# Performance work log

Hardware: AMD Instinct MI355X
Metric: run time of the kernel (lower is better)

## Reference

```python
import jax, jax.numpy as jnp
import numpy as np

N_USERS = 100000
N_ITEMS = 50000
N = N_USERS + N_ITEMS
NNZ = 2400000
D = 64
L = 3
B = 16384


def setup_inputs() -> dict:
    key = jax.random.key(0)
    ks = jax.random.split(key, 12)
    return {
        "user_emb": jax.random.normal(ks[0], (N_USERS, D), jnp.float32) * 0.1,
        "item_emb": jax.random.normal(ks[1], (N_ITEMS, D), jnp.float32) * 0.1,
        "W_gc": jax.random.normal(ks[2], (L, D, D), jnp.float32) * 0.1,
        "b_gc": jax.random.normal(ks[3], (L, 1, D), jnp.float32) * 0.1,
        "W_bi": jax.random.normal(ks[4], (L, D, D), jnp.float32) * 0.1,
        "b_bi": jax.random.normal(ks[5], (L, 1, D), jnp.float32) * 0.1,
        "adj_vals": jax.random.uniform(ks[6], (NNZ,), jnp.float32) * (1.0 / 16.0),
        "adj_rows": jax.random.randint(ks[7], (NNZ,), 0, N, jnp.int32),
        "adj_cols": jax.random.randint(ks[8], (NNZ,), 0, N, jnp.int32),
        "u": jax.random.randint(ks[9], (B,), 0, N_USERS, jnp.int32),
        "i": jax.random.randint(ks[10], (B,), 0, N_ITEMS, jnp.int32),
        "j": jax.random.randint(ks[11], (B,), 0, N_ITEMS, jnp.int32),
    }


def reference(user_emb, item_emb, W_gc, b_gc, W_bi, b_bi, adj_vals, adj_rows, adj_cols, u, i, j):
    n_users = user_emb.shape[0]
    n_nodes = n_users + item_emb.shape[0]
    ego = jnp.concatenate([user_emb, item_emb], axis=0)  # [N, D]
    all_emb = [ego]
    n_layers = W_gc.shape[0]
    for l in range(n_layers):
        # spmm: side = A_hat @ ego  (edge-list gather + weighted segment sum)
        gathered = ego[adj_cols] * adj_vals[:, None]            # [nnz, D]
        side = jax.ops.segment_sum(gathered, adj_rows, num_segments=n_nodes)  # [N, D]
        # graph-conv branch
        sum_emb = jax.nn.leaky_relu(side @ W_gc[l] + b_gc[l], 0.2)
        # bi-interaction branch
        bi_emb = jax.nn.leaky_relu((ego * side) @ W_bi[l] + b_bi[l], 0.2)
        ego = sum_emb + bi_emb
        # L2 normalize per node (F.normalize, eps=1e-12)
        norm = ego / jnp.maximum(jnp.linalg.norm(ego, axis=1, keepdims=True), 1e-12)
        all_emb.append(norm)
    final = jnp.concatenate(all_emb, axis=1)  # [N, D*(L+1)]
    u_g = final[u]
    i_g = final[n_users + i]
    j_g = final[n_users + j]
    return u_g, i_g, j_g
```

## Files before the change

kernel.cpp:

```cpp
#include <hip/hip_runtime.h>

#define DD 64
#define RB 256
#define RB_SHIFT 8
#define CAP 4608
#define NBLKA 512
#define NBLKA_SHIFT 9
#define BMAX 1024
#define COLM 0x3FFFF
#define WT_STRIDE 80
#define EMAX 4704
#define SPAD 68

typedef __attribute__((ext_vector_type(8))) short bf16x8;
typedef __attribute__((ext_vector_type(4))) float f32x4;

static __device__ __forceinline__ float leaky(float x) {
    return x > 0.f ? x : 0.2f * x;
}

static __device__ __forceinline__ unsigned short f2bf(float f) {
    unsigned u = __float_as_uint(f);
    unsigned r = 0x7FFFu + ((u >> 16) & 1u);
    return (unsigned short)((u + r) >> 16);
}
#define BF_LO(w) __int_as_float((int)((w) << 16))
#define BF_HI(w) __int_as_float((int)((w) & 0xFFFF0000u))

static __device__ __forceinline__ bf16x8 pack8(float a, float b, float c, float d,
                                               float e, float f, float g, float h) {
    bf16x8 r;
    r[0] = (short)f2bf(a); r[1] = (short)f2bf(b); r[2] = (short)f2bf(c); r[3] = (short)f2bf(d);
    r[4] = (short)f2bf(e); r[5] = (short)f2bf(f); r[6] = (short)f2bf(g); r[7] = (short)f2bf(h);
    return r;
}

__global__ void concat_kernel(const float4* __restrict__ ue, const float4* __restrict__ ie,
                              float4* __restrict__ ego, ushort4* __restrict__ egob,
                              int n_user4, int total4) {
    int idx = blockIdx.x * blockDim.x + threadIdx.x;
    if (idx >= total4) return;
    float4 v = (idx < n_user4) ? ue[idx] : ie[idx - n_user4];
    ego[idx] = v;
    ushort4 b;
    b.x = f2bf(v.x); b.y = f2bf(v.y); b.z = f2bf(v.z); b.w = f2bf(v.w);
    egob[idx] = b;
}

__global__ void bhist_kernel(const int* __restrict__ rows, int* __restrict__ counts_t, int nnz,
                             int nbuckets) {
    __shared__ int h[BMAX];
    int tid = threadIdx.x, blk = blockIdx.x;
    for (int i = tid; i < nbuckets; i += 256) h[i] = 0;
    __syncthreads();
    int chunk = (nnz + NBLKA - 1) / NBLKA;
    int lo = blk * chunk, hi = min(nnz, lo + chunk);
    for (int e = lo + tid; e < hi; e += 256) atomicAdd(&h[rows[e] >> RB_SHIFT], 1);
    __syncthreads();
    for (int i = tid; i < nbuckets; i += 256) counts_t[blk * nbuckets + i] = h[i];
}

__global__ void scan1_kernel(const int* __restrict__ counts_t, int* __restrict__ offsets,
                             int* __restrict__ blocksums, int flat, int nbuckets) {
    __shared__ int tmp[1024];
    int t = threadIdx.x;
    int g = blockIdx.x * 1024 + t;
    int x = 0;
    if (g < flat) {
        int i = g >> NBLKA_SHIFT, blk = g & (NBLKA - 1);
        x = counts_t[blk * nbuckets + i];
    }
    tmp[t] = x;
    __syncthreads();
    for (int off = 1; off < 1024; off <<= 1) {
        int y = (t >= off) ? tmp[t - off] : 0;
        __syncthreads();
        tmp[t] += y;
        __syncthreads();
    }
    if (g < flat) offsets[g + 1] = tmp[t];
    if (t == 1023) blocksums[blockIdx.x] = tmp[t];
    if (g == 0) offsets[0] = 0;
}

__global__ void scan2_kernel(int* blocksums, int nb) {
    __shared__ int tmp[1024];
    int t = threadIdx.x;
    int v = (t < nb) ? blocksums[t] : 0;
    tmp[t] = v;
    __syncthreads();
    for (int off = 1; off < 1024; off <<= 1) {
        int y = (t >= off) ? tmp[t - off] : 0;
        __syncthreads();
        tmp[t] += y;
        __syncthreads();
    }
    if (t < nb) blocksums[t] = tmp[t] - v;
}

__global__ void scan3_kernel(int* __restrict__ offsets, const int* __restrict__ blocksums,
                             int n) {
    int g = blockIdx.x * 1024 + threadIdx.x;
    if (g < n) offsets[g + 1] += blocksums[blockIdx.x];
}

__global__ void __launch_bounds__(256) bscatter_kernel(
    const int* __restrict__ rows, const int* __restrict__ cols,
    const float* __restrict__ vals, const int* __restrict__ offsets,
    int2* __restrict__ csr_cv, int nnz, int nbuckets) {
    __shared__ int hist[BMAX];
    __shared__ int lbase[BMAX];
    __shared__ int cur[BMAX];
    __shared__ int gcur[BMAX];
    __shared__ int tsum[256];
    __shared__ int2 buf[EMAX];
    __shared__ int dst[EMAX];
    int tid = threadIdx.x, blk = blockIdx.x;
    int chunk = (nnz + NBLKA - 1) / NBLKA;
    int lo = blk * chunk, hi = min(nnz, lo + chunk);
    for (int i = tid; i < BMAX; i += 256)
        gcur[i] = (i < nbuckets) ? offsets[i * NBLKA + blk] : 0;
    for (int sub = lo; sub < hi; sub += EMAX) {
        int scount = min(EMAX, hi - sub);
        for (int i = tid; i < BMAX; i += 256) hist[i] = 0;
        __syncthreads();
        for (int e = sub + tid; e < sub + scount; e += 256)
            atomicAdd(&hist[rows[e] >> RB_SHIFT], 1);
        __syncthreads();
        int loc[4];
        int s = 0;
        int bi = tid * 4;
#pragma unroll
        for (int j = 0; j < 4; ++j) { loc[j] = s; s += hist[bi + j]; }
        tsum[tid] = s;
        __syncthreads();
        for (int off = 1; off < 256; off <<= 1) {
            int v = (tid >= off) ? tsum[tid - off] : 0;
            __syncthreads();
            tsum[tid] += v;
            __syncthreads();
        }
        int excl = tid ? tsum[tid - 1] : 0;
#pragma unroll
        for (int j = 0; j < 4; ++j) {
            lbase[bi + j] = excl + loc[j];
            cur[bi + j] = excl + loc[j];
        }
        __syncthreads();
        for (int e = sub + tid; e < sub + scount; e += 256) {
            int r = rows[e];
            int b = r >> RB_SHIFT;
            int p = atomicAdd(&cur[b], 1);
            int2 cv;
            cv.x = ((r & (RB - 1)) << 18) | cols[e];
            cv.y = __float_as_int(vals[e]);
            buf[p] = cv;
            dst[p] = gcur[b] + (p - lbase[b]);
        }
        __syncthreads();
        for (int k = tid; k < scount; k += 256) csr_cv[dst[k]] = buf[k];
        __syncthreads();
        for (int i = tid; i < BMAX; i += 256) gcur[i] += hist[i];
        __syncthreads();
    }
}

__global__ void __launch_bounds__(256) sort_kernel(
    const int* __restrict__ offsets, const int2* __restrict__ csr_cv,
    int2* __restrict__ sorted_cv, int* __restrict__ rowoff_g, int nnz, int nbuckets) {
    __shared__ int2 sorted[CAP];
    __shared__ int hist[RB];
    __shared__ int rowoff[RB + 1];
    __shared__ int cur[RB];
    int tid = threadIdx.x;
    int b = blockIdx.x;
    int s = offsets[b * NBLKA];
    int e = offsets[(b + 1) * NBLKA];
    int m = e - s;

    hist[tid] = 0;
    __syncthreads();
    for (int k = s + tid; k < e; k += 256)
        atomicAdd(&hist[((unsigned)csr_cv[k].x) >> 18], 1);
    __syncthreads();
    for (int off = 1; off < RB; off <<= 1) {
        int v = (tid >= off) ? hist[tid - off] : 0;
        __syncthreads();
        hist[tid] += v;
        __syncthreads();
    }
    rowoff[tid + 1] = hist[tid];
    if (tid == 0) rowoff[0] = 0;
    __syncthreads();
    cur[tid] = rowoff[tid];
    __syncthreads();
    if (m <= CAP) {
        for (int k = s + tid; k < e; k += 256) {
            int2 cv = csr_cv[k];
            int p = atomicAdd(&cur[((unsigned)cv.x) >> 18], 1);
            sorted[p] = cv;
        }
        __syncthreads();
        for (int k = tid; k < m; k += 256) sorted_cv[s + k] = sorted[k];
    } else {
        for (int k = s + tid; k < e; k += 256) {
            int2 cv = csr_cv[k];
            int p = atomicAdd(&cur[((unsigned)cv.x) >> 18], 1);
            sorted_cv[s + p] = cv;
        }
    }
    rowoff_g[b * RB + tid] = s + rowoff[tid];
    if (b == 0 && tid == 0) rowoff_g[nbuckets * RB] = nnz;
}

#define EDGE8(acc, cvy, g)                                                     \
    do {                                                                       \
        float v_ = __int_as_float(cvy);                                        \
        acc[0] += v_ * BF_LO((g).x); acc[1] += v_ * BF_HI((g).x);              \
        acc[2] += v_ * BF_LO((g).y); acc[3] += v_ * BF_HI((g).y);              \
        acc[4] += v_ * BF_LO((g).z); acc[5] += v_ * BF_HI((g).z);              \
        acc[6] += v_ * BF_LO((g).w); acc[7] += v_ * BF_HI((g).w);              \
    } while (0)

__global__ void __launch_bounds__(256, 4) fused_layer_kernel(
    const uint4* __restrict__ egob_old, const float* __restrict__ ego_old,
    float* __restrict__ ego_new, ushort* __restrict__ egob_new,
    const int* __restrict__ rowoff, const int2* __restrict__ sorted_cv,
    const float* __restrict__ Wgc, const float* __restrict__ bgc,
    const float* __restrict__ Wbi, const float* __restrict__ bbi, int n) {
    __shared__ __align__(16) float sideL[64 * SPAD];
    __shared__ __align__(16) ushort sWg[DD * WT_STRIDE];
    __shared__ __align__(16) ushort sWb[DD * WT_STRIDE];
    int tid = threadIdx.x;
    for (int idx = tid; idx < DD * DD; idx += 256) {
        int k = idx >> 6, c = idx & 63;
        sWg[c * WT_STRIDE + k] = f2bf(Wgc[idx]);
        sWb[c * WT_STRIDE + k] = f2bf(Wbi[idx]);
    }
    int base64 = blockIdx.x * 64;
    int wave = tid >> 6, lane = tid & 63;
    int sub = lane >> 3, l8 = lane & 7;

    int lr0 = wave * 8 + sub;
    int lr1 = lr0 + 32;
    int row0 = base64 + lr0, row1 = base64 + lr1;
    float acc0[8] = {0.f, 0.f, 0.f, 0.f, 0.f, 0.f, 0.f, 0.f};
    float acc1[8] = {0.f, 0.f, 0.f, 0.f, 0.f, 0.f, 0.f, 0.f};
    int k0 = 0, E0 = 0, k1 = 0, E1 = 0;
    if (row0 < n) { k0 = rowoff[row0]; E0 = rowoff[row0 + 1]; }
    if (row1 < n) { k1 = rowoff[row1]; E1 = rowoff[row1 + 1]; }
    int CL0 = (E0 > 0) ? E0 - 1 : 0;
    int CL1 = (E1 > 0) ? E1 - 1 : 0;

    int myit = max((E0 - k0 + 3) >> 2, (E1 - k1 + 3) >> 2);
    myit = max(myit, __shfl_xor(myit, 8, 64));
    myit = max(myit, __shfl_xor(myit, 16, 64));
    myit = max(myit, __shfl_xor(myit, 32, 64));

    int2 cA0[4], cA1[4];
#pragma unroll
    for (int j = 0; j < 4; ++j) {
        int i0 = k0 + j; cA0[j] = sorted_cv[i0 < E0 ? i0 : CL0];
        int i1 = k1 + j; cA1[j] = sorted_cv[i1 < E1 ? i1 : CL1];
    }
    for (int it = 0; it < myit; ++it) {
        uint4 g0[4], g1[4];
#pragma unroll
        for (int j = 0; j < 4; ++j)
            g0[j] = egob_old[(unsigned)(cA0[j].x & COLM) * 8 + l8];
#pragma unroll
        for (int j = 0; j < 4; ++j)
            g1[j] = egob_old[(unsigned)(cA1[j].x & COLM) * 8 + l8];
        int2 cB0[4], cB1[4];
#pragma unroll
        for (int j = 0; j < 4; ++j) {
            int i0 = k0 + 4 + j; cB0[j] = sorted_cv[i0 < E0 ? i0 : CL0];
            int i1 = k1 + 4 + j; cB1[j] = sorted_cv[i1 < E1 ? i1 : CL1];
        }
#pragma unroll
        for (int j = 0; j < 4; ++j) {
            int vb0 = (k0 + j < E0) ? cA0[j].y : 0;
            EDGE8(acc0, vb0, g0[j]);
        }
#pragma unroll
        for (int j = 0; j < 4; ++j) {
            int vb1 = (k1 + j < E1) ? cA1[j].y : 0;
            EDGE8(acc1, vb1, g1[j]);
        }
        k0 += 4; k1 += 4;
#pragma unroll
        for (int j = 0; j < 4; ++j) { cA0[j] = cB0[j]; cA1[j] = cB1[j]; }
    }
    {
        float4 o0 = {acc0[0], acc0[1], acc0[2], acc0[3]};
        float4 o1 = {acc0[4], acc0[5], acc0[6], acc0[7]};
        *(float4*)&sideL[lr0 * SPAD + l8 * 8] = o0;
        *(float4*)&sideL[lr0 * SPAD + l8 * 8 + 4] = o1;
        float4 o2 = {acc1[0], acc1[1], acc1[2], acc1[3]};
        float4 o3 = {acc1[4], acc1[5], acc1[6], acc1[7]};
        *(float4*)&sideL[lr1 * SPAD + l8 * 8] = o2;
        *(float4*)&sideL[lr1 * SPAD + l8 * 8 + 4] = o3;
    }
    __syncthreads();

    int m = lane & 15, quad = lane >> 4;
    int lr = wave * 16 + m;
    int base = base64 + wave * 16;
    int rowc = min(base64 + lr, n - 1);

    float4 s0 = *(const float4*)&sideL[lr * SPAD + quad * 8];
    float4 s1 = *(const float4*)&sideL[lr * SPAD + quad * 8 + 4];
    float4 s2 = *(const float4*)&sideL[lr * SPAD + 32 + quad * 8];
    float4 s3 = *(const float4*)&sideL[lr * SPAD + 32 + quad * 8 + 4];
    const float4* erow = (const float4*)(ego_old + (size_t)rowc * DD);
    float4 e0 = erow[quad * 2], e1 = erow[quad * 2 + 1];
    float4 e2 = erow[8 + quad * 2], e3 = erow[8 + quad * 2 + 1];

    bf16x8 aS_lo = pack8(s0.x, s0.y, s0.z, s0.w, s1.x, s1.y, s1.z, s1.w);
    bf16x8 aS_hi = pack8(s2.x, s2.y, s2.z, s2.w, s3.x, s3.y, s3.z, s3.w);
    bf16x8 aP_lo = pack8(e0.x * s0.x, e0.y * s0.y, e0.z * s0.z, e0.w * s0.w,
                         e1.x * s1.x, e1.y * s1.y, e1.z * s1.z, e1.w * s1.w);
    bf16x8 aP_hi = pack8(e2.x * s2.x, e2.y * s2.y, e2.z * s2.z, e2.w * s2.w,
                         e3.x * s3.x, e3.y * s3.y, e3.z * s3.z, e3.w * s3.w);

    f32x4 accG[4], accB[4];
#pragma unroll
    for (int ct = 0; ct < 4; ++ct) {
        accG[ct] = (f32x4){0.f, 0.f, 0.f, 0.f};
        accB[ct] = (f32x4){0.f, 0.f, 0.f, 0.f};
    }
#pragma unroll
    for (int ct = 0; ct < 4; ++ct) {
        int col = ct * 16 + m;
        bf16x8 bg_lo = *(const bf16x8*)&sWg[col * WT_STRIDE + quad * 8];
        bf16x8 bg_hi = *(const bf16x8*)&sWg[col * WT_STRIDE + 32 + quad * 8];
        bf16x8 bb_lo = *(const bf16x8*)&sWb[col * WT_STRIDE + quad * 8];
        bf16x8 bb_hi = *(const bf16x8*)&sWb[col * WT_STRIDE + 32 + quad * 8];
        accG[ct] = __builtin_amdgcn_mfma_f32_16x16x32_bf16(aS_lo, bg_lo, accG[ct], 0, 0, 0);
        accG[ct] = __builtin_amdgcn_mfma_f32_16x16x32_bf16(aS_hi, bg_hi, accG[ct], 0, 0, 0);
        accB[ct] = __builtin_amdgcn_mfma_f32_16x16x32_bf16(aP_lo, bb_lo, accB[ct], 0, 0, 0);
        accB[ct] = __builtin_amdgcn_mfma_f32_16x16x32_bf16(aP_hi, bb_hi, accB[ct], 0, 0, 0);
    }

#pragma unroll
    for (int ct = 0; ct < 4; ++ct) {
        int col = ct * 16 + m;
        float bg = bgc[col], bb = bbi[col];
#pragma unroll
        for (int r = 0; r < 4; ++r) {
            int node = base + quad * 4 + r;
            if (node < n) {
                float o = leaky(accG[ct][r] + bg) + leaky(accB[ct][r] + bb);
                ego_new[(size_t)node * DD + col] = o;
                egob_new[(size_t)node * DD + col] = f2bf(o);
            }
        }
    }
}

__global__ void gather_kernel(const float* __restrict__ ego, const int* __restrict__ u,
                              const int* __restrict__ ii, const int* __restrict__ jj,
                              float* __restrict__ out, int layer, int B, int n_users,
                              int normalize) {
    int wid = (blockIdx.x * blockDim.x + threadIdx.x) >> 6;
    int lane = threadIdx.x & 63;
    if (wid >= 3 * B) return;
    int arr = wid / B;
    int b = wid - arr * B;
    int node = (arr == 0) ? u[b] : ((arr == 1) ? n_users + ii[b] : n_users + jj[b]);
    float v = ego[node * DD + lane];
    if (normalize) {
        float ss = v * v;
#pragma unroll
        for (int m = 32; m; m >>= 1) ss += __shfl_xor(ss, m, 64);
        v /= fmaxf(sqrtf(ss), 1e-12f);
    }
    out[wid * 256 + layer * DD + lane] = v;
}

extern "C" void kernel_launch(void* const* d_in, const int* in_sizes, int n_in,
                              void* d_out, int out_size, void* d_ws, size_t ws_size,
                              hipStream_t stream) {
    const float* user_emb = (const float*)d_in[0];
    const float* item_emb = (const float*)d_in[1];
    const float* W_gc = (const float*)d_in[2];
    const float* b_gc = (const float*)d_in[3];
    const float* W_bi = (const float*)d_in[4];
    const float* b_bi = (const float*)d_in[5];
    const float* adj_vals = (const float*)d_in[6];
    const int* adj_rows = (const int*)d_in[7];
    const int* adj_cols = (const int*)d_in[8];
    const int* u = (const int*)d_in[9];
    const int* ii = (const int*)d_in[10];
    const int* jj = (const int*)d_in[11];
    float* out = (float*)d_out;

    const int D = DD;
    int n_users = in_sizes[0] / D;
    int n_items = in_sizes[1] / D;
    int n = n_users + n_items;
    int nnz = in_sizes[6];
    int B = in_sizes[9];
    int L = in_sizes[2] / (D * D);

    int nbuckets = (n + RB - 1) / RB;
    int flat = nbuckets * NBLKA;

    char* ws = (char*)d_ws;
    auto alloc = [&](size_t bytes) {
        char* p = ws;
        ws += (bytes + 255) & ~(size_t)255;
        return p;
    };
    float* ego_a = (float*)alloc((size_t)n * D * 4);
    float* ego_b = (float*)alloc((size_t)n * D * 4);
    ushort* egob_a = (ushort*)alloc((size_t)n * D * 2);
    ushort* egob_b = (ushort*)alloc((size_t)n * D * 2);
    int* counts_t = (int*)alloc((size_t)flat * 4);
    int* offsets = (int*)alloc((size_t)(flat + 1) * 4);
    int* blocksums = (int*)alloc(4096);
    int2* csr_cv = (int2*)alloc((size_t)nnz * 8);
    int2* sorted_cv = (int2*)alloc((size_t)nnz * 8);
    int* rowoff = (int*)alloc((size_t)(nbuckets * RB + 1) * 4);

    int total4 = n * D / 4, nu4 = n_users * D / 4;
    concat_kernel<<<(total4 + 255) / 256, 256, 0, stream>>>(
        (const float4*)user_emb, (const float4*)item_emb, (float4*)ego_a, (ushort4*)egob_a,
        nu4, total4);

    int grows = 3 * B;
    gather_kernel<<<(grows + 3) / 4, 256, 0, stream>>>(ego_a, u, ii, jj, out, 0, B, n_users, 0);

    bhist_kernel<<<NBLKA, 256, 0, stream>>>(adj_rows, counts_t, nnz, nbuckets);
    int nblk1 = (flat + 1023) / 1024;
    scan1_kernel<<<nblk1, 1024, 0, stream>>>(counts_t, offsets, blocksums, flat, nbuckets);
    scan2_kernel<<<1, 1024, 0, stream>>>(blocksums, nblk1);
    scan3_kernel<<<nblk1, 1024, 0, stream>>>(offsets, blocksums, flat);
    bscatter_kernel<<<NBLKA, 256, 0, stream>>>(adj_rows, adj_cols, adj_vals, offsets, csr_cv,
                                               nnz, nbuckets);
    sort_kernel<<<nbuckets, 256, 0, stream>>>(offsets, csr_cv, sorted_cv, rowoff, nnz, nbuckets);

    float* eo = ego_a; ushort* ebo = egob_a;
    float* en = ego_b; ushort* ebn = egob_b;
    int fblocks = (n + 63) / 64;
    for (int l = 0; l < L; ++l) {
        fused_layer_kernel<<<fblocks, 256, 0, stream>>>(
            (const uint4*)ebo, eo, en, ebn, rowoff, sorted_cv,
            W_gc + (size_t)l * D * D, b_gc + (size_t)l * D,
            W_bi + (size_t)l * D * D, b_bi + (size_t)l * D, n);
        gather_kernel<<<(grows + 3) / 4, 256, 0, stream>>>(en, u, ii, jj, out, l + 1, B,
                                                           n_users, 1);
        float* tf = eo; eo = en; en = tf;
        ushort* tb = ebo; ebo = ebn; ebn = tb;
    }
}
```

Baseline: 458.1 us.

## Replace bucketed two-pass CSR build with global atomic count and scatter

```diff
diff --git a/kernel.cpp b/kernel.cpp
--- a/kernel.cpp
+++ b/kernel.cpp
@@ -1,15 +1,8 @@
 #include <hip/hip_runtime.h>
 
 #define DD 64
-#define RB 256
-#define RB_SHIFT 8
-#define CAP 4608
-#define NBLKA 512
-#define NBLKA_SHIFT 9
-#define BMAX 1024
 #define COLM 0x3FFFF
 #define WT_STRIDE 80
-#define EMAX 4704
 #define SPAD 68
 
 typedef __attribute__((ext_vector_type(8))) short bf16x8;
@@ -47,29 +40,18 @@
     egob[idx] = b;
 }
 
-__global__ void bhist_kernel(const int* __restrict__ rows, int* __restrict__ counts_t, int nnz,
-                             int nbuckets) {
-    __shared__ int h[BMAX];
-    int tid = threadIdx.x, blk = blockIdx.x;
-    for (int i = tid; i < nbuckets; i += 256) h[i] = 0;
-    __syncthreads();
-    int chunk = (nnz + NBLKA - 1) / NBLKA;
-    int lo = blk * chunk, hi = min(nnz, lo + chunk);
-    for (int e = lo + tid; e < hi; e += 256) atomicAdd(&h[rows[e] >> RB_SHIFT], 1);
-    __syncthreads();
-    for (int i = tid; i < nbuckets; i += 256) counts_t[blk * nbuckets + i] = h[i];
-}
-
-__global__ void scan1_kernel(const int* __restrict__ counts_t, int* __restrict__ offsets,
-                             int* __restrict__ blocksums, int flat, int nbuckets) {
+__global__ void count_kernel(const int* __restrict__ rows, int* __restrict__ counts, int nnz) {
+    int i = blockIdx.x * blockDim.x + threadIdx.x;
+    int stride = gridDim.x * blockDim.x;
+    for (int e = i; e < nnz; e += stride) atomicAdd(&counts[rows[e]], 1);
+}
+
+__global__ void scanL1_kernel(const int* __restrict__ counts, int* __restrict__ offsets,
+                              int* __restrict__ blocksums, int n) {
     __shared__ int tmp[1024];
     int t = threadIdx.x;
     int g = blockIdx.x * 1024 + t;
-    int x = 0;
-    if (g < flat) {
-        int i = g >> NBLKA_SHIFT, blk = g & (NBLKA - 1);
-        x = counts_t[blk * nbuckets + i];
-    }
+    int x = (g < n) ? counts[g] : 0;
     tmp[t] = x;
     __syncthreads();
     for (int off = 1; off < 1024; off <<= 1) {
@@ -78,7 +60,7 @@
         tmp[t] += y;
         __syncthreads();
     }
-    if (g < flat) offsets[g + 1] = tmp[t];
+    if (g < n) offsets[g + 1] = tmp[t];
     if (t == 1023) blocksums[blockIdx.x] = tmp[t];
     if (g == 0) offsets[0] = 0;
 }
@@ -104,113 +86,20 @@
     if (g < n) offsets[g + 1] += blocksums[blockIdx.x];
 }
 
-__global__ void __launch_bounds__(256) bscatter_kernel(
-    const int* __restrict__ rows, const int* __restrict__ cols,
-    const float* __restrict__ vals, const int* __restrict__ offsets,
-    int2* __restrict__ csr_cv, int nnz, int nbuckets) {
-    __shared__ int hist[BMAX];
-    __shared__ int lbase[BMAX];
-    __shared__ int cur[BMAX];
-    __shared__ int gcur[BMAX];
-    __shared__ int tsum[256];
-    __shared__ int2 buf[EMAX];
-    __shared__ int dst[EMAX];
-    int tid = threadIdx.x, blk = blockIdx.x;
-    int chunk = (nnz + NBLKA - 1) / NBLKA;
-    int lo = blk * chunk, hi = min(nnz, lo + chunk);
-    for (int i = tid; i < BMAX; i += 256)
-        gcur[i] = (i < nbuckets) ? offsets[i * NBLKA + blk] : 0;
-    for (int sub = lo; sub < hi; sub += EMAX) {
-        int scount = min(EMAX, hi - sub);
-        for (int i = tid; i < BMAX; i += 256) hist[i] = 0;
-        __syncthreads();
-        for (int e = sub + tid; e < sub + scount; e += 256)
-            atomicAdd(&hist[rows[e] >> RB_SHIFT], 1);
-        __syncthreads();
-        int loc[4];
-        int s = 0;
-        int bi = tid * 4;
-#pragma unroll
-        for (int j = 0; j < 4; ++j) { loc[j] = s; s += hist[bi + j]; }
-        tsum[tid] = s;
-        __syncthreads();
-        for (int off = 1; off < 256; off <<= 1) {
-            int v = (tid >= off) ? tsum[tid - off] : 0;
-            __syncthreads();
-            tsum[tid] += v;
-            __syncthreads();
-        }
-        int excl = tid ? tsum[tid - 1] : 0;
-#pragma unroll
-        for (int j = 0; j < 4; ++j) {
-            lbase[bi + j] = excl + loc[j];
-            cur[bi + j] = excl + loc[j];
-        }
-        __syncthreads();
-        for (int e = sub + tid; e < sub + scount; e += 256) {
-            int r = rows[e];
-            int b = r >> RB_SHIFT;
-            int p = atomicAdd(&cur[b], 1);
-            int2 cv;
-            cv.x = ((r & (RB - 1)) << 18) | cols[e];
-            cv.y = __float_as_int(vals[e]);
-            buf[p] = cv;
-            dst[p] = gcur[b] + (p - lbase[b]);
-        }
-        __syncthreads();
-        for (int k = tid; k < scount; k += 256) csr_cv[dst[k]] = buf[k];
-        __syncthreads();
-        for (int i = tid; i < BMAX; i += 256) gcur[i] += hist[i];
-        __syncthreads();
-    }
-}
-
-__global__ void __launch_bounds__(256) sort_kernel(
-    const int* __restrict__ offsets, const int2* __restrict__ csr_cv,
-    int2* __restrict__ sorted_cv, int* __restrict__ rowoff_g, int nnz, int nbuckets) {
-    __shared__ int2 sorted[CAP];
-    __shared__ int hist[RB];
-    __shared__ int rowoff[RB + 1];
-    __shared__ int cur[RB];
-    int tid = threadIdx.x;
-    int b = blockIdx.x;
-    int s = offsets[b * NBLKA];
-    int e = offsets[(b + 1) * NBLKA];
-    int m = e - s;
-
-    hist[tid] = 0;
-    __syncthreads();
-    for (int k = s + tid; k < e; k += 256)
-        atomicAdd(&hist[((unsigned)csr_cv[k].x) >> 18], 1);
-    __syncthreads();
-    for (int off = 1; off < RB; off <<= 1) {
-        int v = (tid >= off) ? hist[tid - off] : 0;
-        __syncthreads();
-        hist[tid] += v;
-        __syncthreads();
-    }
-    rowoff[tid + 1] = hist[tid];
-    if (tid == 0) rowoff[0] = 0;
-    __syncthreads();
-    cur[tid] = rowoff[tid];
-    __syncthreads();
-    if (m <= CAP) {
-        for (int k = s + tid; k < e; k += 256) {
-            int2 cv = csr_cv[k];
-            int p = atomicAdd(&cur[((unsigned)cv.x) >> 18], 1);
-            sorted[p] = cv;
-        }
-        __syncthreads();
-        for (int k = tid; k < m; k += 256) sorted_cv[s + k] = sorted[k];
-    } else {
-        for (int k = s + tid; k < e; k += 256) {
-            int2 cv = csr_cv[k];
-            int p = atomicAdd(&cur[((unsigned)cv.x) >> 18], 1);
-            sorted_cv[s + p] = cv;
-        }
-    }
-    rowoff_g[b * RB + tid] = s + rowoff[tid];
-    if (b == 0 && tid == 0) rowoff_g[nbuckets * RB] = nnz;
+__global__ void scatter_kernel(const int* __restrict__ rows, const int* __restrict__ cols,
+                               const float* __restrict__ vals, const int* __restrict__ rowoff,
+                               int* __restrict__ cursor, int2* __restrict__ sorted_cv,
+                               int nnz) {
+    int i = blockIdx.x * blockDim.x + threadIdx.x;
+    int stride = gridDim.x * blockDim.x;
+    for (int e = i; e < nnz; e += stride) {
+        int r = rows[e];
+        int p = atomicAdd(&cursor[r], 1);
+        int2 cv;
+        cv.x = cols[e];
+        cv.y = __float_as_int(vals[e]);
+        sorted_cv[rowoff[r] + p] = cv;
+    }
 }
 
 #define EDGE8(acc, cvy, g)                                                     \
@@ -233,9 +122,9 @@
     __shared__ __align__(16) ushort sWb[DD * WT_STRIDE];
     int tid = threadIdx.x;
     for (int idx = tid; idx < DD * DD; idx += 256) {
-        int k = idx >> 6, c = idx & 63;
-        sWg[c * WT_STRIDE + k] = f2bf(Wgc[idx]);
-        sWb[c * WT_STRIDE + k] = f2bf(Wbi[idx]);
+        int k = idx & 63, c = idx >> 6;
+        sWg[c * WT_STRIDE + k] = f2bf(Wgc[k * 64 + c]);
+        sWb[c * WT_STRIDE + k] = f2bf(Wbi[k * 64 + c]);
     }
     int base64 = blockIdx.x * 64;
     int wave = tid >> 6, lane = tid & 63;
@@ -403,9 +292,6 @@
     int B = in_sizes[9];
     int L = in_sizes[2] / (D * D);
 
-    int nbuckets = (n + RB - 1) / RB;
-    int flat = nbuckets * NBLKA;
-
     char* ws = (char*)d_ws;
     auto alloc = [&](size_t bytes) {
         char* p = ws;
@@ -416,12 +302,14 @@
     float* ego_b = (float*)alloc((size_t)n * D * 4);
     ushort* egob_a = (ushort*)alloc((size_t)n * D * 2);
     ushort* egob_b = (ushort*)alloc((size_t)n * D * 2);
-    int* counts_t = (int*)alloc((size_t)flat * 4);
-    int* offsets = (int*)alloc((size_t)(flat + 1) * 4);
+    int* counts = (int*)alloc((size_t)n * 4);
+    int* cursor = (int*)alloc((size_t)n * 4);
     int* blocksums = (int*)alloc(4096);
-    int2* csr_cv = (int2*)alloc((size_t)nnz * 8);
+    int* rowoff = (int*)alloc((size_t)(n + 1) * 4);
     int2* sorted_cv = (int2*)alloc((size_t)nnz * 8);
-    int* rowoff = (int*)alloc((size_t)(nbuckets * RB + 1) * 4);
+
+    hipMemsetAsync(counts, 0, (size_t)n * 4, stream);
+    hipMemsetAsync(cursor, 0, (size_t)n * 4, stream);
 
     int total4 = n * D / 4, nu4 = n_users * D / 4;
     concat_kernel<<<(total4 + 255) / 256, 256, 0, stream>>>(
@@ -431,14 +319,13 @@
     int grows = 3 * B;
     gather_kernel<<<(grows + 3) / 4, 256, 0, stream>>>(ego_a, u, ii, jj, out, 0, B, n_users, 0);
 
-    bhist_kernel<<<NBLKA, 256, 0, stream>>>(adj_rows, counts_t, nnz, nbuckets);
-    int nblk1 = (flat + 1023) / 1024;
-    scan1_kernel<<<nblk1, 1024, 0, stream>>>(counts_t, offsets, blocksums, flat, nbuckets);
-    scan2_kernel<<<1, 1024, 0, stream>>>(blocksums, nblk1);
-    scan3_kernel<<<nblk1, 1024, 0, stream>>>(offsets, blocksums, flat);
-    bscatter_kernel<<<NBLKA, 256, 0, stream>>>(adj_rows, adj_cols, adj_vals, offsets, csr_cv,
-                                               nnz, nbuckets);
-    sort_kernel<<<nbuckets, 256, 0, stream>>>(offsets, csr_cv, sorted_cv, rowoff, nnz, nbuckets);
+    count_kernel<<<1024, 256, 0, stream>>>(adj_rows, counts, nnz);
+    int nblk = (n + 1023) / 1024;
+    scanL1_kernel<<<nblk, 1024, 0, stream>>>(counts, rowoff, blocksums, n);
+    scan2_kernel<<<1, 1024, 0, stream>>>(blocksums, nblk);
+    scan3_kernel<<<nblk, 1024, 0, stream>>>(rowoff, blocksums, n);
+    scatter_kernel<<<1024, 256, 0, stream>>>(adj_rows, adj_cols, adj_vals, rowoff, cursor,
+                                             sorted_cv, nnz);
 
     float* eo = ego_a; ushort* ebo = egob_a;
     float* en = ego_b; ushort* ebn = egob_b;
```

After: 695.2 us. 1.52x slower.
